# Kernel optimization log

Measured on AMD Instinct MI355X. Metric: run time of the kernel, lower is better.

The kernel has to match this reference:

```python
import jax, jax.numpy as jnp
import numpy as np

N = 1024
H = 128
W = 128
TANX = 0.5
TANY = 0.5
FX = W / (2.0 * TANX)
FY = H / (2.0 * TANY)
SCALE_MOD = 1.0

# spherical-harmonic constants (match 3DGS CUDA)
C0 = 0.28209479177387814
C1 = 0.4886025119029199
C2 = (1.0925484305920792, -1.0925484305920792, 0.31539156525252005, -1.0925484305920792, 0.5462742152960396)
C3 = (-0.5900435899266435, 2.890611442640554, -0.4570457994644658, 0.3731763325901154, -0.4570457994644658, 1.445305721320277, -0.5900435899266435)


def _quat_to_rot(q):
    q = q / jnp.linalg.norm(q, axis=-1, keepdims=True)
    r, x, y, z = q[:, 0], q[:, 1], q[:, 2], q[:, 3]
    row0 = jnp.stack([1 - 2 * (y * y + z * z), 2 * (x * y - r * z), 2 * (x * z + r * y)], -1)
    row1 = jnp.stack([2 * (x * y + r * z), 1 - 2 * (x * x + z * z), 2 * (y * z - r * x)], -1)
    row2 = jnp.stack([2 * (x * z - r * y), 2 * (y * z + r * x), 1 - 2 * (x * x + y * y)], -1)
    return jnp.stack([row0, row1, row2], 1)  # [n,3,3]


def _sh_to_rgb(sh, d):
    x, y, z = d[:, 0:1], d[:, 1:2], d[:, 2:3]
    res = C0 * sh[:, 0]
    res = res - C1 * y * sh[:, 1] + C1 * z * sh[:, 2] - C1 * x * sh[:, 3]
    xx, yy, zz = x * x, y * y, z * z
    xy, yz, xz = x * y, y * z, x * z
    res = (res + C2[0] * xy * sh[:, 4] + C2[1] * yz * sh[:, 5]
           + C2[2] * (2 * zz - xx - yy) * sh[:, 6] + C2[3] * xz * sh[:, 7]
           + C2[4] * (xx - yy) * sh[:, 8])
    res = (res + C3[0] * y * (3 * xx - yy) * sh[:, 9] + C3[1] * xy * z * sh[:, 10]
           + C3[2] * y * (4 * zz - xx - yy) * sh[:, 11]
           + C3[3] * z * (2 * zz - 3 * xx - 3 * yy) * sh[:, 12]
           + C3[4] * x * (4 * zz - xx - yy) * sh[:, 13]
           + C3[5] * z * (xx - yy) * sh[:, 14] + C3[6] * x * (xx - 3 * yy) * sh[:, 15])
    return jnp.maximum(res + 0.5, 0.0)


def _rasterize(means3D, opacities, shs, scales, rotations, viewmatrix, projmatrix, campos, bg):
    n = means3D.shape[0]
    dt = means3D.dtype
    hom = jnp.concatenate([means3D, jnp.ones((n, 1), dt)], -1)
    p_view = hom @ viewmatrix                      # row-vector convention
    depth = p_view[:, 2]
    valid = depth > 0.2
    p_hom = hom @ projmatrix
    p_proj = p_hom[:, :3] / (p_hom[:, 3:4] + 1e-7)
    # 3D covariance: Sigma = R diag(s^2) R^T
    R = _quat_to_rot(rotations)
    M = R * (scales * SCALE_MOD)[:, None, :]
    Sigma = jnp.einsum('nij,nkj->nik', M, M)
    # EWA projection to 2D covariance
    tz = jnp.where(valid, depth, 1.0)
    txtz = jnp.clip(p_view[:, 0] / tz, -1.3 * TANX, 1.3 * TANX) * tz
    tytz = jnp.clip(p_view[:, 1] / tz, -1.3 * TANY, 1.3 * TANY) * tz
    zero = jnp.zeros_like(tz)
    J = jnp.stack([
        jnp.stack([FX / tz, zero, -FX * txtz / (tz * tz)], -1),
        jnp.stack([zero, FY / tz, -FY * tytz / (tz * tz)], -1)], 1)  # [n,2,3]
    Wr = viewmatrix[:3, :3].T
    T2 = jnp.einsum('nij,jk->nik', J, Wr)
    cov2 = jnp.einsum('nij,njk,nlk->nil', T2, Sigma, T2)
    a = cov2[:, 0, 0] + 0.3
    b = cov2[:, 0, 1]
    c = cov2[:, 1, 1] + 0.3
    det = a * c - b * b
    valid = valid & (det > 0)
    inv_det = 1.0 / jnp.where(det > 0, det, 1.0)
    conA, conB, conC = c * inv_det, -b * inv_det, a * inv_det
    mid = 0.5 * (a + c)
    lam1 = mid + jnp.sqrt(jnp.maximum(0.1, mid * mid - det))
    radii = jnp.where(valid, jnp.ceil(3.0 * jnp.sqrt(lam1)), 0.0).astype(jnp.int32)
    # NDC -> pixel centers (ndc2Pix)
    xy = ((p_proj[:, :2] + 1.0) * jnp.array([W, H], dt) - 1.0) * 0.5
    # SH evaluation -> RGB
    dirs = means3D - campos[None, :]
    dirs = dirs / jnp.linalg.norm(dirs, axis=-1, keepdims=True)
    colors = _sh_to_rgb(shs, dirs)                 # [n,3]
    # global front-to-back depth sort
    order = jnp.argsort(jnp.where(valid, depth, jnp.inf))
    conA, conB, conC = conA[order], conB[order], conC[order]
    xyo = xy[order]
    opo = opacities[order, 0]
    colo = colors[order]
    vo = valid[order]
    # dense per-pixel evaluation (tile binning is a perf optimization only)
    yy, xx = jnp.meshgrid(jnp.arange(H, dtype=dt), jnp.arange(W, dtype=dt), indexing='ij')
    pxf = xx.reshape(-1)
    pyf = yy.reshape(-1)
    dx = xyo[:, 0:1] - pxf[None, :]                # [n, HW]
    dy = xyo[:, 1:2] - pyf[None, :]
    power = -0.5 * (conA[:, None] * dx * dx + conC[:, None] * dy * dy) - conB[:, None] * dx * dy
    alpha = jnp.minimum(0.99, opo[:, None] * jnp.exp(jnp.minimum(power, 0.0)))
    alpha = jnp.where((power <= 0) & (alpha >= 1.0 / 255.0) & vo[:, None], alpha, 0.0)
    Tinc = jnp.cumprod(1.0 - alpha, axis=0)        # T after gaussian i
    Texc = jnp.concatenate([jnp.ones((1, H * W), dt), Tinc[:-1]], 0)  # T before gaussian i
    ae = jnp.where(Tinc >= 1e-4, alpha, 0.0)       # early-termination threshold as in CUDA
    weight = Texc * ae
    img = jnp.einsum('np,nc->cp', weight, colo)
    Tfin = jnp.prod(1.0 - ae, axis=0)
    img = img + bg[:, None] * Tfin[None, :]
    return img.reshape(3, H, W), radii


def setup_inputs() -> dict:
    key = jax.random.key(0)
    ks = jax.random.split(key, 6)
    means3D = jax.random.uniform(ks[0], (N, 3)) * jnp.array([4.0, 4.0, 4.0]) + jnp.array([-2.0, -2.0, 2.0])
    means2D = jnp.zeros((N, 3), jnp.float32)
    opacities = jax.random.uniform(ks[1], (N, 1)) * 0.8 + 0.2
    shs = jax.random.normal(ks[2], (N, 16, 3)) * 0.3
    scales = jax.random.uniform(ks[3], (N, 3)) * 0.1 + 0.02
    rotations = jax.random.normal(ks[4], (N, 4))
    viewmatrix = jnp.eye(4, dtype=jnp.float32)     # camera at origin looking +z
    znear, zfar = 0.01, 100.0
    projmatrix = jnp.array([[1.0 / TANX, 0, 0, 0],
                            [0, 1.0 / TANY, 0, 0],
                            [0, 0, zfar / (zfar - znear), 1.0],
                            [0, 0, -zfar * znear / (zfar - znear), 0]], jnp.float32)
    campos = jnp.zeros(3, jnp.float32)
    bg = jnp.zeros(3, jnp.float32)
    return {"means3D": means3D, "means2D": means2D, "opacities": opacities, "shs": shs,
            "scales": scales, "rotations": rotations, "viewmatrix": viewmatrix,
            "projmatrix": projmatrix, "campos": campos, "bg": bg}


def reference(means3D, means2D, opacities, shs, scales, rotations, viewmatrix, projmatrix, campos, bg):
    color, radii = _rasterize(means3D, opacities, shs, scales, rotations, viewmatrix, projmatrix, campos, bg)
    return color, radii
```

## Files before the change

kernel.cpp:

```cpp
#include <hip/hip_runtime.h>
#include <stdint.h>

#define N_G   1024
#define H_IMG 128
#define W_IMG 128
#define TILE  8
#define TILES_X (W_IMG / TILE)
#define N_TILES (TILES_X * (H_IMG/TILE))
#define FXc   128.0f
#define FYc   128.0f

#define WS_PAYLOAD 0
#define WS_CULL    (N_G*12)
#define WS_KEYS    (N_G*12 + N_G*4)

__global__ __launch_bounds__(64) void prep_kernel(
    const float* __restrict__ means3D, const float* __restrict__ opac,
    const float* __restrict__ shs,     const float* __restrict__ scales,
    const float* __restrict__ rot,     const float* __restrict__ vm,
    const float* __restrict__ pm,      const float* __restrict__ campos,
    float* __restrict__ radii_out,     float* __restrict__ payload,
    float4* __restrict__ cull,         unsigned long long* __restrict__ keys)
{
    const int n = blockIdx.x * 64 + threadIdx.x;
    if (n >= N_G) return;

    float mx = means3D[n*3+0], my = means3D[n*3+1], mz = means3D[n*3+2];

    float pv0   = mx*vm[0] + my*vm[4] + mz*vm[8]  + vm[12];
    float pv1   = mx*vm[1] + my*vm[5] + mz*vm[9]  + vm[13];
    float depth = mx*vm[2] + my*vm[6] + mz*vm[10] + vm[14];
    bool dvalid = depth > 0.2f;

    float ph0 = mx*pm[0] + my*pm[4] + mz*pm[8]  + pm[12];
    float ph1 = mx*pm[1] + my*pm[5] + mz*pm[9]  + pm[13];
    float ph3 = mx*pm[3] + my*pm[7] + mz*pm[11] + pm[15];
    float invw = 1.0f / (ph3 + 1e-7f);
    float pp0 = ph0 * invw, pp1 = ph1 * invw;

    float q0 = rot[n*4+0], q1 = rot[n*4+1], q2 = rot[n*4+2], q3 = rot[n*4+3];
    float qn = sqrtf(q0*q0 + q1*q1 + q2*q2 + q3*q3);
    float qr = q0/qn, qx = q1/qn, qy = q2/qn, qz = q3/qn;
    float R00 = 1.f - 2.f*(qy*qy + qz*qz), R01 = 2.f*(qx*qy - qr*qz), R02 = 2.f*(qx*qz + qr*qy);
    float R10 = 2.f*(qx*qy + qr*qz), R11 = 1.f - 2.f*(qx*qx + qz*qz), R12 = 2.f*(qy*qz - qr*qx);
    float R20 = 2.f*(qx*qz - qr*qy), R21 = 2.f*(qy*qz + qr*qx), R22 = 1.f - 2.f*(qx*qx + qy*qy);

    float s0 = scales[n*3+0], s1 = scales[n*3+1], s2 = scales[n*3+2];
    float M00=R00*s0, M01=R01*s1, M02=R02*s2;
    float M10=R10*s0, M11=R11*s1, M12=R12*s2;
    float M20=R20*s0, M21=R21*s1, M22=R22*s2;

    float S00 = M00*M00 + M01*M01 + M02*M02;
    float S01 = M00*M10 + M01*M11 + M02*M12;
    float S02 = M00*M20 + M01*M21 + M02*M22;
    float S11 = M10*M10 + M11*M11 + M12*M12;
    float S12 = M10*M20 + M11*M21 + M12*M22;
    float S22 = M20*M20 + M21*M21 + M22*M22;

    float tz   = dvalid ? depth : 1.0f;
    float txtz = fminf(fmaxf(pv0 / tz, -0.65f), 0.65f) * tz;
    float tytz = fminf(fmaxf(pv1 / tz, -0.65f), 0.65f) * tz;
    float J00 = FXc / tz, J02 = -FXc * txtz / (tz*tz);
    float J11 = FYc / tz, J12 = -FYc * tytz / (tz*tz);

    float T20k0 = J00*vm[0] + J02*vm[2];
    float T20k1 = J00*vm[4] + J02*vm[6];
    float T20k2 = J00*vm[8] + J02*vm[10];
    float T21k0 = J11*vm[1] + J12*vm[2];
    float T21k1 = J11*vm[5] + J12*vm[6];
    float T21k2 = J11*vm[9] + J12*vm[10];

    float U00 = T20k0*S00 + T20k1*S01 + T20k2*S02;
    float U01 = T20k0*S01 + T20k1*S11 + T20k2*S12;
    float U02 = T20k0*S02 + T20k1*S12 + T20k2*S22;
    float U10 = T21k0*S00 + T21k1*S01 + T21k2*S02;
    float U11 = T21k0*S01 + T21k1*S11 + T21k2*S12;
    float U12 = T21k0*S02 + T21k1*S12 + T21k2*S22;
    float cov00 = U00*T20k0 + U01*T20k1 + U02*T20k2;
    float cov01 = U00*T21k0 + U01*T21k1 + U02*T21k2;
    float cov11 = U10*T21k0 + U11*T21k1 + U12*T21k2;

    float a = cov00 + 0.3f, b = cov01, c = cov11 + 0.3f;
    float det = a*c - b*b;
    bool valid = dvalid && (det > 0.0f);
    float inv_det = (det > 0.0f) ? (1.0f / det) : 1.0f;
    float conA = c * inv_det, conB = -b * inv_det, conC = a * inv_det;

    float mid  = 0.5f * (a + c);
    float lam1 = mid + sqrtf(fmaxf(0.1f, mid*mid - det));
    radii_out[n] = valid ? ceilf(3.0f * sqrtf(lam1)) : 0.0f;

    float gx = ((pp0 + 1.0f) * (float)W_IMG - 1.0f) * 0.5f;
    float gy = ((pp1 + 1.0f) * (float)H_IMG - 1.0f) * 0.5f;

    float dxm = mx - campos[0], dym = my - campos[1], dzm = mz - campos[2];
    float dn = sqrtf(dxm*dxm + dym*dym + dzm*dzm);
    float sx = dxm/dn, sy = dym/dn, sz = dzm/dn;
    float xx = sx*sx, yy = sy*sy, zz = sz*sz;
    float xy = sx*sy, yz = sy*sz, xz = sx*sz;
    const float* sh = shs + n*48;
    float col[3];
    #pragma unroll
    for (int ch = 0; ch < 3; ++ch) {
        float res = 0.28209479177387814f * sh[0*3+ch]
            - 0.4886025119029199f * sy * sh[1*3+ch]
            + 0.4886025119029199f * sz * sh[2*3+ch]
            - 0.4886025119029199f * sx * sh[3*3+ch]
            + 1.0925484305920792f  * xy * sh[4*3+ch]
            + (-1.0925484305920792f) * yz * sh[5*3+ch]
            + 0.31539156525252005f * (2.f*zz - xx - yy) * sh[6*3+ch]
            + (-1.0925484305920792f) * xz * sh[7*3+ch]
            + 0.5462742152960396f  * (xx - yy) * sh[8*3+ch]
            + (-0.5900435899266435f) * sy * (3.f*xx - yy) * sh[9*3+ch]
            + 2.890611442640554f   * xy * sz * sh[10*3+ch]
            + (-0.4570457994644658f) * sy * (4.f*zz - xx - yy) * sh[11*3+ch]
            + 0.3731763325901154f  * sz * (2.f*zz - 3.f*xx - 3.f*yy) * sh[12*3+ch]
            + (-0.4570457994644658f) * sx * (4.f*zz - xx - yy) * sh[13*3+ch]
            + 1.445305721320277f   * sz * (xx - yy) * sh[14*3+ch]
            + (-0.5900435899266435f) * sx * (xx - 3.f*yy) * sh[15*3+ch];
        col[ch] = fmaxf(res + 0.5f, 0.0f);
    }

    float op = opac[n];
    float* pl = payload + n*12;
    pl[0]=gx; pl[1]=gy; pl[2]=conA; pl[3]=conB; pl[4]=conC; pl[5]=op;
    pl[6]=col[0]; pl[7]=col[1]; pl[8]=col[2]; pl[9]=0.f; pl[10]=0.f; pl[11]=0.f;

    float op255 = op * 255.0f;
    float rc2 = (valid && op255 > 1.0f) ? (2.0f * logf(op255) * lam1 * 1.01f + 1.0f)
                                        : -1.0f;
    cull[n] = make_float4(gx, gy, rc2, 0.0f);

    unsigned int kb = __float_as_uint(depth);
    keys[n] = ((unsigned long long)kb << 32) | (unsigned int)n;
}

__global__ __launch_bounds__(64) void raster_tile(
    const float* __restrict__ payload,
    const float4* __restrict__ cull,
    const unsigned long long* __restrict__ keys,
    const float* __restrict__ bg,
    float* __restrict__ out)
{
    __shared__ unsigned long long list[N_G];
    __shared__ float batch[64 * 12];
    __shared__ int cnt;

    const int lane = threadIdx.x;
    const int tile = blockIdx.x;
    const int tx = tile & (TILES_X - 1), ty = tile / TILES_X;
    const float x0 = (float)(tx * TILE), x1 = x0 + (float)(TILE - 1);
    const float y0 = (float)(ty * TILE), y1 = y0 + (float)(TILE - 1);

    if (lane == 0) cnt = 0;
    __syncthreads();

    for (int i = lane; i < N_G; i += 64) {
        float4 ci = cull[i];
        float cx = fminf(fmaxf(ci.x, x0), x1) - ci.x;
        float cy = fminf(fmaxf(ci.y, y0), y1) - ci.y;
        if (cx*cx + cy*cy <= ci.z) {
            int slot = atomicAdd(&cnt, 1);
            list[slot] = keys[i];
        }
    }
    __syncthreads();
    const int M = cnt;

    int P = 1; while (P < M) P <<= 1;
    for (int i = M + lane; i < P; i += 64) list[i] = ~0ull;
    __syncthreads();
    for (int k = 2; k <= P; k <<= 1) {
        for (int j = k >> 1; j > 0; j >>= 1) {
            for (int i = lane; i < P; i += 64) {
                int l = i ^ j;
                if (l > i) {
                    unsigned long long ka = list[i], kb = list[l];
                    bool asc = ((i & k) == 0);
                    if ((ka > kb) == asc) { list[i] = kb; list[l] = ka; }
                }
            }
            __syncthreads();
        }
    }

    const float px = x0 + (float)(lane & (TILE - 1));
    const float py = y0 + (float)(lane / TILE);
    float T = 1.0f, Tfin = 1.0f, cr = 0.f, cg = 0.f, cb = 0.f;
    bool live = true;

    for (int base = 0; base < M; base += 64) {
        if (__ballot(live) == 0ull) break;
        int nb = min(64, M - base);
        if (lane < nb) {
            int idx = (int)(list[base + lane] & 0xFFFFFFFFu);
            const float4* pp = (const float4*)(payload + idx * 12);
            float4 p0 = pp[0], p1 = pp[1], p2 = pp[2];
            float4* bp = (float4*)(batch + lane * 12);
            bp[0] = p0; bp[1] = p1; bp[2] = p2;
        }
        __syncthreads();
        for (int j = 0; j < nb; ++j) {
            float4 g0 = *(const float4*)(batch + j * 12);
            float4 g1 = *(const float4*)(batch + j * 12 + 4);
            float  b2 = batch[j * 12 + 8];
            float dx = g0.x - px, dy = g0.y - py;
            float power = -0.5f * (g0.z*dx*dx + g1.x*dy*dy) - g0.w*dx*dy;
            float alpha = fminf(0.99f, g1.y * expf(power));
            if (live && power <= 0.0f && alpha >= (1.0f/255.0f)) {
                float Tnew = T * (1.0f - alpha);
                if (Tnew < 1e-4f) {
                    live = false;
                } else {
                    float w = T * alpha;
                    cr += w * g1.z; cg += w * g1.w; cb += w * b2;
                    Tfin *= (1.0f - alpha);
                    T = Tnew;
                }
            }
        }
        __syncthreads();
    }

    int p = (int)py * W_IMG + (int)px;
    out[p]                 = cr + bg[0] * Tfin;
    out[H_IMG*W_IMG + p]   = cg + bg[1] * Tfin;
    out[2*H_IMG*W_IMG + p] = cb + bg[2] * Tfin;
}

extern "C" void kernel_launch(void* const* d_in, const int* in_sizes, int n_in,
                              void* d_out, int out_size, void* d_ws, size_t ws_size,
                              hipStream_t stream) {
    const float* means3D = (const float*)d_in[0];
    const float* opac    = (const float*)d_in[2];
    const float* shs     = (const float*)d_in[3];
    const float* scales  = (const float*)d_in[4];
    const float* rot     = (const float*)d_in[5];
    const float* vm      = (const float*)d_in[6];
    const float* pm      = (const float*)d_in[7];
    const float* campos  = (const float*)d_in[8];
    const float* bg      = (const float*)d_in[9];

    float* out = (float*)d_out;
    float* wsf = (float*)d_ws;
    float*              payload = wsf + WS_PAYLOAD;
    float4*             cullv   = (float4*)(wsf + WS_CULL);
    unsigned long long* keys    = (unsigned long long*)(wsf + WS_KEYS);

    prep_kernel<<<N_G/64, 64, 0, stream>>>(means3D, opac, shs, scales, rot,
                                           vm, pm, campos,
                                           out + 3*H_IMG*W_IMG,
                                           payload, cullv, keys);
    raster_tile<<<N_TILES, 64, 0, stream>>>(payload, cullv, keys, bg, out);
}
```

Before: 93.99 us.

## Replace per-tile bitonic sort with one global rank sort and streamed culling

Each tile no longer culls and bitonic-sorts its own list in shared memory. A new kernel ranks all gaussians once by depth (O(N^2) comparisons, invalid ones keyed to +inf) and scatters their payload into sorted order. Each raster tile then streams the sorted payload in chunks of 64, culls with a wave ballot and compacts the survivors into shared memory, prefetching the next chunk while it works. This removes the many per-tile sort barriers at the cost of an extra launch and every tile reading all 1024 entries. Prep also switches to 256-thread blocks and vectorized float4 loads for the rotation and SH inputs.

```diff
diff --git a/kernel.cpp b/kernel.cpp
--- a/kernel.cpp
+++ b/kernel.cpp
@@ -10,19 +10,19 @@
 #define FXc   128.0f
 #define FYc   128.0f
 
-#define WS_PAYLOAD 0
-#define WS_CULL    (N_G*12)
-#define WS_KEYS    (N_G*12 + N_G*4)
-
-__global__ __launch_bounds__(64) void prep_kernel(
+#define WS_PAY    0
+#define WS_SORTED (N_G*12)
+#define WS_KEYS   (N_G*24)
+
+__global__ __launch_bounds__(256) void prep_kernel(
     const float* __restrict__ means3D, const float* __restrict__ opac,
     const float* __restrict__ shs,     const float* __restrict__ scales,
     const float* __restrict__ rot,     const float* __restrict__ vm,
     const float* __restrict__ pm,      const float* __restrict__ campos,
-    float* __restrict__ radii_out,     float* __restrict__ payload,
-    float4* __restrict__ cull,         unsigned long long* __restrict__ keys)
+    float* __restrict__ radii_out,     float4* __restrict__ payload,
+    unsigned long long* __restrict__ keys)
 {
-    const int n = blockIdx.x * 64 + threadIdx.x;
+    const int n = blockIdx.x * 256 + threadIdx.x;
     if (n >= N_G) return;
 
     float mx = means3D[n*3+0], my = means3D[n*3+1], mz = means3D[n*3+2];
@@ -38,9 +38,9 @@
     float invw = 1.0f / (ph3 + 1e-7f);
     float pp0 = ph0 * invw, pp1 = ph1 * invw;
 
-    float q0 = rot[n*4+0], q1 = rot[n*4+1], q2 = rot[n*4+2], q3 = rot[n*4+3];
-    float qn = sqrtf(q0*q0 + q1*q1 + q2*q2 + q3*q3);
-    float qr = q0/qn, qx = q1/qn, qy = q2/qn, qz = q3/qn;
+    float4 q = *(const float4*)(rot + n*4);
+    float qn = sqrtf(q.x*q.x + q.y*q.y + q.z*q.z + q.w*q.w);
+    float qr = q.x/qn, qx = q.y/qn, qy = q.z/qn, qz = q.w/qn;
     float R00 = 1.f - 2.f*(qy*qy + qz*qz), R01 = 2.f*(qx*qy - qr*qz), R02 = 2.f*(qx*qz + qr*qy);
     float R10 = 2.f*(qx*qy + qr*qz), R11 = 1.f - 2.f*(qx*qx + qz*qz), R12 = 2.f*(qy*qz - qr*qx);
     float R20 = 2.f*(qx*qz - qr*qy), R21 = 2.f*(qy*qz + qr*qx), R22 = 1.f - 2.f*(qx*qx + qy*qy);
@@ -98,128 +98,131 @@
     float sx = dxm/dn, sy = dym/dn, sz = dzm/dn;
     float xx = sx*sx, yy = sy*sy, zz = sz*sz;
     float xy = sx*sy, yz = sy*sz, xz = sx*sz;
-    const float* sh = shs + n*48;
+    const float4* sh4 = (const float4*)(shs + n*48);
+    float shf[48];
+    #pragma unroll
+    for (int k = 0; k < 12; ++k) {
+        float4 v = sh4[k];
+        shf[k*4+0]=v.x; shf[k*4+1]=v.y; shf[k*4+2]=v.z; shf[k*4+3]=v.w;
+    }
     float col[3];
     #pragma unroll
     for (int ch = 0; ch < 3; ++ch) {
-        float res = 0.28209479177387814f * sh[0*3+ch]
-            - 0.4886025119029199f * sy * sh[1*3+ch]
-            + 0.4886025119029199f * sz * sh[2*3+ch]
-            - 0.4886025119029199f * sx * sh[3*3+ch]
-            + 1.0925484305920792f  * xy * sh[4*3+ch]
-            + (-1.0925484305920792f) * yz * sh[5*3+ch]
-            + 0.31539156525252005f * (2.f*zz - xx - yy) * sh[6*3+ch]
-            + (-1.0925484305920792f) * xz * sh[7*3+ch]
-            + 0.5462742152960396f  * (xx - yy) * sh[8*3+ch]
-            + (-0.5900435899266435f) * sy * (3.f*xx - yy) * sh[9*3+ch]
-            + 2.890611442640554f   * xy * sz * sh[10*3+ch]
-            + (-0.4570457994644658f) * sy * (4.f*zz - xx - yy) * sh[11*3+ch]
-            + 0.3731763325901154f  * sz * (2.f*zz - 3.f*xx - 3.f*yy) * sh[12*3+ch]
-            + (-0.4570457994644658f) * sx * (4.f*zz - xx - yy) * sh[13*3+ch]
-            + 1.445305721320277f   * sz * (xx - yy) * sh[14*3+ch]
-            + (-0.5900435899266435f) * sx * (xx - 3.f*yy) * sh[15*3+ch];
+        float res = 0.28209479177387814f * shf[0*3+ch]
+            - 0.4886025119029199f * sy * shf[1*3+ch]
+            + 0.4886025119029199f * sz * shf[2*3+ch]
+            - 0.4886025119029199f * sx * shf[3*3+ch]
+            + 1.0925484305920792f  * xy * shf[4*3+ch]
+            + (-1.0925484305920792f) * yz * shf[5*3+ch]
+            + 0.31539156525252005f * (2.f*zz - xx - yy) * shf[6*3+ch]
+            + (-1.0925484305920792f) * xz * shf[7*3+ch]
+            + 0.5462742152960396f  * (xx - yy) * shf[8*3+ch]
+            + (-0.5900435899266435f) * sy * (3.f*xx - yy) * shf[9*3+ch]
+            + 2.890611442640554f   * xy * sz * shf[10*3+ch]
+            + (-0.4570457994644658f) * sy * (4.f*zz - xx - yy) * shf[11*3+ch]
+            + 0.3731763325901154f  * sz * (2.f*zz - 3.f*xx - 3.f*yy) * shf[12*3+ch]
+            + (-0.4570457994644658f) * sx * (4.f*zz - xx - yy) * shf[13*3+ch]
+            + 1.445305721320277f   * sz * (xx - yy) * shf[14*3+ch]
+            + (-0.5900435899266435f) * sx * (xx - 3.f*yy) * shf[15*3+ch];
         col[ch] = fmaxf(res + 0.5f, 0.0f);
     }
 
     float op = opac[n];
-    float* pl = payload + n*12;
-    pl[0]=gx; pl[1]=gy; pl[2]=conA; pl[3]=conB; pl[4]=conC; pl[5]=op;
-    pl[6]=col[0]; pl[7]=col[1]; pl[8]=col[2]; pl[9]=0.f; pl[10]=0.f; pl[11]=0.f;
-
     float op255 = op * 255.0f;
     float rc2 = (valid && op255 > 1.0f) ? (2.0f * logf(op255) * lam1 * 1.01f + 1.0f)
                                         : -1.0f;
-    cull[n] = make_float4(gx, gy, rc2, 0.0f);
-
-    unsigned int kb = __float_as_uint(depth);
+
+    payload[n*3+0] = make_float4(gx, gy, conA, conB);
+    payload[n*3+1] = make_float4(conC, op, col[0], col[1]);
+    payload[n*3+2] = make_float4(col[2], rc2, 0.f, 0.f);
+
+    unsigned int kb = valid ? __float_as_uint(depth) : 0x7F800000u;
     keys[n] = ((unsigned long long)kb << 32) | (unsigned int)n;
 }
 
+__global__ __launch_bounds__(256) void rank_sort_kernel(
+    const unsigned long long* __restrict__ keys,
+    const float4* __restrict__ payload,
+    float4* __restrict__ sorted_payload)
+{
+    const int n = blockIdx.x * 256 + threadIdx.x;
+    if (n >= N_G) return;
+    unsigned long long mine = keys[n];
+    int rank = 0;
+    #pragma unroll 8
+    for (int j = 0; j < N_G; ++j)
+        rank += (keys[j] < mine) ? 1 : 0;
+    float4 p0 = payload[n*3+0], p1 = payload[n*3+1], p2 = payload[n*3+2];
+    sorted_payload[rank*3+0] = p0;
+    sorted_payload[rank*3+1] = p1;
+    sorted_payload[rank*3+2] = p2;
+}
+
 __global__ __launch_bounds__(64) void raster_tile(
-    const float* __restrict__ payload,
-    const float4* __restrict__ cull,
-    const unsigned long long* __restrict__ keys,
+    const float4* __restrict__ pay,
     const float* __restrict__ bg,
     float* __restrict__ out)
 {
-    __shared__ unsigned long long list[N_G];
-    __shared__ float batch[64 * 12];
-    __shared__ int cnt;
+    __shared__ float batch[64 * 16];
 
     const int lane = threadIdx.x;
     const int tile = blockIdx.x;
     const int tx = tile & (TILES_X - 1), ty = tile / TILES_X;
     const float x0 = (float)(tx * TILE), x1 = x0 + (float)(TILE - 1);
     const float y0 = (float)(ty * TILE), y1 = y0 + (float)(TILE - 1);
-
-    if (lane == 0) cnt = 0;
-    __syncthreads();
-
-    for (int i = lane; i < N_G; i += 64) {
-        float4 ci = cull[i];
-        float cx = fminf(fmaxf(ci.x, x0), x1) - ci.x;
-        float cy = fminf(fmaxf(ci.y, y0), y1) - ci.y;
-        if (cx*cx + cy*cy <= ci.z) {
-            int slot = atomicAdd(&cnt, 1);
-            list[slot] = keys[i];
+    const float px = x0 + (float)(lane & (TILE - 1));
+    const float py = y0 + (float)(lane / TILE);
+
+    float T = 1.0f, Tfin = 1.0f, cr = 0.f, cg = 0.f, cb = 0.f;
+    bool live = true;
+
+    float4 a0 = pay[lane*3+0], a1 = pay[lane*3+1], a2 = pay[lane*3+2];
+
+    for (int base = 0; base < N_G; base += 64) {
+        float4 n0, n1, n2;
+        const bool more = (base + 64) < N_G;
+        if (more) {
+            const float4* np = pay + (base + 64 + lane) * 3;
+            n0 = np[0]; n1 = np[1]; n2 = np[2];
         }
-    }
-    __syncthreads();
-    const int M = cnt;
-
-    int P = 1; while (P < M) P <<= 1;
-    for (int i = M + lane; i < P; i += 64) list[i] = ~0ull;
-    __syncthreads();
-    for (int k = 2; k <= P; k <<= 1) {
-        for (int j = k >> 1; j > 0; j >>= 1) {
-            for (int i = lane; i < P; i += 64) {
-                int l = i ^ j;
-                if (l > i) {
-                    unsigned long long ka = list[i], kb = list[l];
-                    bool asc = ((i & k) == 0);
-                    if ((ka > kb) == asc) { list[i] = kb; list[l] = ka; }
+
+        float cx = fminf(fmaxf(a0.x, x0), x1) - a0.x;
+        float cy = fminf(fmaxf(a0.y, y0), y1) - a0.y;
+        bool pass = (cx*cx + cy*cy) <= a2.y;
+        unsigned long long mask = __ballot(pass);
+
+        if (mask != 0ull) {
+            int pos = __popcll(mask & ((1ull << lane) - 1ull));
+            if (pass) {
+                float4* bp = (float4*)(batch + pos * 16);
+                bp[0] = a0; bp[1] = a1; bp[2] = a2;
+            }
+            __syncthreads();
+            int nb = __popcll(mask);
+            for (int j = 0; j < nb; ++j) {
+                float4 g0 = *(const float4*)(batch + j * 16);
+                float4 g1 = *(const float4*)(batch + j * 16 + 4);
+                float  b2 = batch[j * 16 + 8];
+                float dx = g0.x - px, dy = g0.y - py;
+                float power = -0.5f * (g0.z*dx*dx + g1.x*dy*dy) - g0.w*dx*dy;
+                float alpha = fminf(0.99f, g1.y * expf(power));
+                if (live && power <= 0.0f && alpha >= (1.0f/255.0f)) {
+                    float Tnew = T * (1.0f - alpha);
+                    if (Tnew < 1e-4f) {
+                        live = false;
+                    } else {
+                        float w = T * alpha;
+                        cr += w * g1.z; cg += w * g1.w; cb += w * b2;
+                        Tfin *= (1.0f - alpha);
+                        T = Tnew;
+                    }
                 }
             }
             __syncthreads();
+            if (__ballot(live) == 0ull) break;
         }
-    }
-
-    const float px = x0 + (float)(lane & (TILE - 1));
-    const float py = y0 + (float)(lane / TILE);
-    float T = 1.0f, Tfin = 1.0f, cr = 0.f, cg = 0.f, cb = 0.f;
-    bool live = true;
-
-    for (int base = 0; base < M; base += 64) {
-        if (__ballot(live) == 0ull) break;
-        int nb = min(64, M - base);
-        if (lane < nb) {
-            int idx = (int)(list[base + lane] & 0xFFFFFFFFu);
-            const float4* pp = (const float4*)(payload + idx * 12);
-            float4 p0 = pp[0], p1 = pp[1], p2 = pp[2];
-            float4* bp = (float4*)(batch + lane * 12);
-            bp[0] = p0; bp[1] = p1; bp[2] = p2;
-        }
-        __syncthreads();
-        for (int j = 0; j < nb; ++j) {
-            float4 g0 = *(const float4*)(batch + j * 12);
-            float4 g1 = *(const float4*)(batch + j * 12 + 4);
-            float  b2 = batch[j * 12 + 8];
-            float dx = g0.x - px, dy = g0.y - py;
-            float power = -0.5f * (g0.z*dx*dx + g1.x*dy*dy) - g0.w*dx*dy;
-            float alpha = fminf(0.99f, g1.y * expf(power));
-            if (live && power <= 0.0f && alpha >= (1.0f/255.0f)) {
-                float Tnew = T * (1.0f - alpha);
-                if (Tnew < 1e-4f) {
-                    live = false;
-                } else {
-                    float w = T * alpha;
-                    cr += w * g1.z; cg += w * g1.w; cb += w * b2;
-                    Tfin *= (1.0f - alpha);
-                    T = Tnew;
-                }
-            }
-        }
-        __syncthreads();
+
+        a0 = n0; a1 = n1; a2 = n2;
     }
 
     int p = (int)py * W_IMG + (int)px;
@@ -243,13 +246,13 @@
 
     float* out = (float*)d_out;
     float* wsf = (float*)d_ws;
-    float*              payload = wsf + WS_PAYLOAD;
-    float4*             cullv   = (float4*)(wsf + WS_CULL);
+    float4*             payload = (float4*)(wsf + WS_PAY);
+    float4*             sorted  = (float4*)(wsf + WS_SORTED);
     unsigned long long* keys    = (unsigned long long*)(wsf + WS_KEYS);
 
-    prep_kernel<<<N_G/64, 64, 0, stream>>>(means3D, opac, shs, scales, rot,
-                                           vm, pm, campos,
-                                           out + 3*H_IMG*W_IMG,
-                                           payload, cullv, keys);
-    raster_tile<<<N_TILES, 64, 0, stream>>>(payload, cullv, keys, bg, out);
-}
+    prep_kernel<<<N_G/256, 256, 0, stream>>>(means3D, opac, shs, scales, rot,
+                                             vm, pm, campos,
+                                             out + 3*H_IMG*W_IMG, payload, keys);
+    rank_sort_kernel<<<N_G/256, 256, 0, stream>>>(keys, payload, sorted);
+    raster_tile<<<N_TILES, 64, 0, stream>>>(sorted, bg, out);
+}
```

New measurement: 132.3 us. 40.7% more time.
